# Optimization experiments

Hardware: AMD Instinct MI355X
Metric: run time of the kernel (lower is better)

## Reference

```python
import jax, jax.numpy as jnp
import numpy as np

C = 64
DQK = C // 8  # query/key channels


def setup_inputs() -> dict:
    key = jax.random.key(0)
    ks = jax.random.split(key, 8)
    B, H, W = 4, 64, 64
    x = jax.random.normal(ks[0], (B, C, H, W), dtype=jnp.float32)
    # 1x1 conv weights stored as (out_ch, in_ch); biases as (out_ch,)
    wq = jax.random.normal(ks[1], (DQK, C), dtype=jnp.float32) * 0.05
    bq = jnp.zeros((DQK,), dtype=jnp.float32)
    wk = jax.random.normal(ks[2], (DQK, C), dtype=jnp.float32) * 0.05
    bk = jnp.zeros((DQK,), dtype=jnp.float32)
    wv = jax.random.normal(ks[3], (C, C), dtype=jnp.float32) * 0.05
    bv = jnp.zeros((C,), dtype=jnp.float32)
    gamma = jnp.zeros((1,), dtype=jnp.float32)
    return {"x": x, "wq": wq, "bq": bq, "wk": wk, "bk": bk,
            "wv": wv, "bv": bv, "gamma": gamma}


def reference(x, wq, bq, wk, bk, wv, bv, gamma):
    B, Cc, H, W = x.shape
    N = H * W
    xf = x.reshape(B, Cc, N)  # (B, C, N)
    # 1x1 convs == channel-wise matmuls
    q = jnp.einsum('oc,bcn->bon', wq, xf) + bq[None, :, None]  # (B, dqk, N)
    k = jnp.einsum('oc,bcn->bon', wk, xf) + bk[None, :, None]  # (B, dqk, N)
    v = jnp.einsum('oc,bcn->bon', wv, xf) + bv[None, :, None]  # (B, C, N)
    # qk = q^T k -> (B, N, N), softmax over last dim
    qk = jnp.einsum('bdn,bdm->bnm', q, k)
    attn = jax.nn.softmax(qk, axis=-1)
    # out = v @ attn^T : out[b,c,i] = sum_j v[b,c,j] * attn[b,i,j]
    out = jnp.einsum('bcj,bij->bci', v, attn)
    out = out.reshape(B, Cc, H, W)
    return gamma * out + x
```

## Files before the change

kernel.cpp:

```cpp
#include <hip/hip_runtime.h>
#include <cmath>

namespace {

constexpr int B = 4;
constexpr int C = 64;
constexpr int N = 4096;
constexpr float LOG2E = 1.4426950408889634f;

typedef __bf16 bf16x8 __attribute__((ext_vector_type(8)));
typedef float f32x16 __attribute__((ext_vector_type(16)));
typedef unsigned short u16;

union B8 {
  int4 i;
  bf16x8 h;
  unsigned int w[4];
};

__device__ inline u16 f2bf(float f) {
  unsigned int u = __float_as_uint(f);
  u += 0x7FFFu + ((u >> 16) & 1u);
  return (u16)(u >> 16);
}

__device__ inline unsigned int cvt_pk_bf16(float lo, float hi) {
  unsigned int r;
  asm("v_cvt_pk_bf16_f32 %0, %1, %2" : "=v"(r) : "v"(lo), "v"(hi));
  return r;
}

__device__ inline float exp2_fast(float x) {
#if __has_builtin(__builtin_amdgcn_exp2f)
  return __builtin_amdgcn_exp2f(x);
#else
  return exp2f(x);
#endif
}

__device__ inline void pl32_swap(unsigned int& a, unsigned int& b) {
#if __has_builtin(__builtin_amdgcn_permlane32_swap)
  auto r = __builtin_amdgcn_permlane32_swap(a, b, false, false);
  a = (unsigned int)r[0];
  b = (unsigned int)r[1];
#else
  asm volatile("s_nop 1\n\tv_permlane32_swap_b32 %0, %1" : "+v"(a), "+v"(b));
#endif
}

__global__ __launch_bounds__(256) void qkv_kernel(
    const float* __restrict__ x,
    const float* __restrict__ wq, const float* __restrict__ bq,
    const float* __restrict__ wk, const float* __restrict__ bk,
    const float* __restrict__ wv, const float* __restrict__ bv,
    u16* __restrict__ qt, u16* __restrict__ kt, u16* __restrict__ vo) {
  const int bid = blockIdx.x;
  const int xcd = bid & 7;
  const int b = xcd >> 1;
  const int cg = (bid >> 3) & 3;
  const int nt = (xcd & 1) * 32 + (bid >> 5);
  const int t = threadIdx.x;
  const int nn = t & 63;
  const int wid = __builtin_amdgcn_readfirstlane(t >> 6);
  const int n = nt * 64 + nn;
  const float* xb = x + (size_t)b * C * N + n;

  const int c0 = cg * 16 + wid * 4;
  float a0 = bv[c0], a1 = bv[c0 + 1], a2 = bv[c0 + 2], a3 = bv[c0 + 3];

  if (cg == 0) {
    const int o0 = wid * 2;
    float qa0 = bq[o0], qa1 = bq[o0 + 1];
    float ka0 = bk[o0], ka1 = bk[o0 + 1];
    #pragma unroll 8
    for (int c = 0; c < C; ++c) {
      const float xv = xb[(size_t)c * N];
      a0 = fmaf(wv[(c0 + 0) * C + c], xv, a0);
      a1 = fmaf(wv[(c0 + 1) * C + c], xv, a1);
      a2 = fmaf(wv[(c0 + 2) * C + c], xv, a2);
      a3 = fmaf(wv[(c0 + 3) * C + c], xv, a3);
      qa0 = fmaf(wq[o0 * C + c], xv, qa0);
      qa1 = fmaf(wq[(o0 + 1) * C + c], xv, qa1);
      ka0 = fmaf(wk[o0 * C + c], xv, ka0);
      ka1 = fmaf(wk[(o0 + 1) * C + c], xv, ka1);
    }
    const unsigned int qw =
        (unsigned int)f2bf(qa0 * LOG2E) | ((unsigned int)f2bf(qa1 * LOG2E) << 16);
    const unsigned int kw =
        (unsigned int)f2bf(ka0) | ((unsigned int)f2bf(ka1) << 16);
    *reinterpret_cast<unsigned int*>(qt + ((size_t)b * N + n) * 8 + o0) = qw;
    *reinterpret_cast<unsigned int*>(kt + ((size_t)b * N + n) * 8 + o0) = kw;
  } else {
    #pragma unroll 8
    for (int c = 0; c < C; ++c) {
      const float xv = xb[(size_t)c * N];
      a0 = fmaf(wv[(c0 + 0) * C + c], xv, a0);
      a1 = fmaf(wv[(c0 + 1) * C + c], xv, a1);
      a2 = fmaf(wv[(c0 + 2) * C + c], xv, a2);
      a3 = fmaf(wv[(c0 + 3) * C + c], xv, a3);
    }
  }

  const size_t tb = ((size_t)b * (N / 16) + (n >> 4)) * (C * 16) + (n & 15);
  vo[tb + (size_t)(c0 + 0) * 16] = f2bf(a0);
  vo[tb + (size_t)(c0 + 1) * 16] = f2bf(a1);
  vo[tb + (size_t)(c0 + 2) * 16] = f2bf(a2);
  vo[tb + (size_t)(c0 + 3) * 16] = f2bf(a3);
}

__global__ __launch_bounds__(512, 4) void attn_kernel(
    const u16* __restrict__ qt, const u16* __restrict__ kt,
    const u16* __restrict__ vv, const float* __restrict__ x,
    const float* __restrict__ gamma, float* __restrict__ out) {
  const int bid = blockIdx.x;
  const int xcd = bid & 7;
  const int b = xcd >> 1;
  const int i0 = ((xcd & 1) * 64 + (bid >> 3)) * 32;
  const int t = threadIdx.x;
  const int lane = t & 63;
  const int w = __builtin_amdgcn_readfirstlane(t >> 6);
  const int il = lane & 31;
  const int hi = lane >> 5;

  __shared__ float l_lds[8][32];
  __shared__ u16 o_lds[8][32][66];

  B8 qf;
  if (hi == 0)
    qf.i = *reinterpret_cast<const int4*>(qt + ((size_t)b * N + i0 + il) * 8);
  else
    qf.i = make_int4(0, 0, 0, 0);

  const u16* ktb = kt + (size_t)b * N * 8;
  const u16* vbase = vv + (size_t)b * (N / 16) * (C * 16) + il * 16 + hi * 8;

  f32x16 accA, accB, zero16;
  #pragma unroll
  for (int r = 0; r < 16; ++r) { accA[r] = 0.f; accB[r] = 0.f; zero16[r] = 0.f; }
  float lrun = 0.f;

  B8 kfA, va0A, va1A, vb0A, vb1A;
  B8 kfB, va0B, va1B, vb0B, vb1B;

  auto LOAD = [&](int jt, B8& kf, B8& va0, B8& va1, B8& vb0, B8& vb1) {
    const int j0 = w * 512 + jt * 32;
    if (hi == 0)
      kf.i = *reinterpret_cast<const int4*>(ktb + (size_t)(j0 + il) * 8);
    else
      kf.i = make_int4(0, 0, 0, 0);
    const u16* vp = vbase + (size_t)(j0 >> 4) * (C * 16);
    va0.i = *reinterpret_cast<const int4*>(vp);
    va1.i = *reinterpret_cast<const int4*>(vp + 1024);
    vb0.i = *reinterpret_cast<const int4*>(vp + 512);
    vb1.i = *reinterpret_cast<const int4*>(vp + 1536);
  };

  auto COMPUTE = [&](const B8& kf, const B8& va0, const B8& va1, const B8& vb0,
                     const B8& vb1) {
    f32x16 S = __builtin_amdgcn_mfma_f32_32x32x16_bf16(kf.h, qf.h, zero16, 0, 0, 0);
    float p[16];
    #pragma unroll
    for (int r = 0; r < 16; ++r) p[r] = exp2_fast(S[r]);
    const float t0 = (p[0] + p[1]) + (p[2] + p[3]);
    const float t1 = (p[4] + p[5]) + (p[6] + p[7]);
    const float t2 = (p[8] + p[9]) + (p[10] + p[11]);
    const float t3 = (p[12] + p[13]) + (p[14] + p[15]);
    lrun += (t0 + t1) + (t2 + t3);
    B8 pf0, pf1;
    {
      unsigned a0 = cvt_pk_bf16(p[0], p[1]);
      unsigned a1 = cvt_pk_bf16(p[2], p[3]);
      unsigned b0 = cvt_pk_bf16(p[4], p[5]);
      unsigned b1 = cvt_pk_bf16(p[6], p[7]);
      pl32_swap(a0, b0);
      pl32_swap(a1, b1);
      pf0.w[0] = a0; pf0.w[1] = a1; pf0.w[2] = b0; pf0.w[3] = b1;
      a0 = cvt_pk_bf16(p[8], p[9]);
      a1 = cvt_pk_bf16(p[10], p[11]);
      b0 = cvt_pk_bf16(p[12], p[13]);
      b1 = cvt_pk_bf16(p[14], p[15]);
      pl32_swap(a0, b0);
      pl32_swap(a1, b1);
      pf1.w[0] = a0; pf1.w[1] = a1; pf1.w[2] = b0; pf1.w[3] = b1;
    }
    accA = __builtin_amdgcn_mfma_f32_32x32x16_bf16(va0.h, pf0.h, accA, 0, 0, 0);
    accA = __builtin_amdgcn_mfma_f32_32x32x16_bf16(va1.h, pf1.h, accA, 0, 0, 0);
    accB = __builtin_amdgcn_mfma_f32_32x32x16_bf16(vb0.h, pf0.h, accB, 0, 0, 0);
    accB = __builtin_amdgcn_mfma_f32_32x32x16_bf16(vb1.h, pf1.h, accB, 0, 0, 0);
  };

  LOAD(0, kfA, va0A, va1A, vb0A, vb1A);
  #pragma unroll 1
  for (int it = 0; it < 8; ++it) {
    LOAD(2 * it + 1, kfB, va0B, va1B, vb0B, vb1B);
    COMPUTE(kfA, va0A, va1A, vb0A, vb1A);
    if (it < 7) LOAD(2 * it + 2, kfA, va0A, va1A, vb0A, vb1A);
    COMPUTE(kfB, va0B, va1B, vb0B, vb1B);
  }

  const float lw = lrun + __shfl_xor(lrun, 32);
  if (hi == 0) l_lds[w][il] = lw;
  #pragma unroll
  for (int r = 0; r < 16; r += 2) {
    const int c = (r & 3) + 8 * (r >> 2) + 4 * hi;
    *reinterpret_cast<unsigned int*>(&o_lds[w][il][c]) =
        cvt_pk_bf16(accA[r], accA[r + 1]);
    *reinterpret_cast<unsigned int*>(&o_lds[w][il][c + 32]) =
        cvt_pk_bf16(accB[r], accB[r + 1]);
  }
  __syncthreads();

  const int i = t & 31;
  float Li = 0.f;
  #pragma unroll
  for (int ww = 0; ww < 8; ++ww) Li += l_lds[ww][i];
  const float ginv = gamma[0] / Li;

  #pragma unroll
  for (int q4 = 0; q4 < 4; ++q4) {
    const int flat = t + q4 * 512;
    const int c = flat >> 5;
    float s = 0.f;
    #pragma unroll
    for (int ww = 0; ww < 8; ++ww)
      s += __uint_as_float((unsigned int)o_lds[ww][i][c] << 16);
    const size_t off = ((size_t)b * C + c) * N + i0 + i;
    out[off] = fmaf(ginv, s, x[off]);
  }
}

}

extern "C" void kernel_launch(void* const* d_in, const int* in_sizes, int n_in,
                              void* d_out, int out_size, void* d_ws, size_t ws_size,
                              hipStream_t stream) {
  const float* x     = (const float*)d_in[0];
  const float* wq    = (const float*)d_in[1];
  const float* bq    = (const float*)d_in[2];
  const float* wk    = (const float*)d_in[3];
  const float* bk    = (const float*)d_in[4];
  const float* wv    = (const float*)d_in[5];
  const float* bv    = (const float*)d_in[6];
  const float* gamma = (const float*)d_in[7];
  float* out = (float*)d_out;

  u16* qt = (u16*)d_ws;
  u16* kt = qt + (size_t)B * N * 8;
  u16* vo = kt + (size_t)B * N * 8;

  qkv_kernel<<<B * 64 * 4, 256, 0, stream>>>(x, wq, bq, wk, bk, wv, bv, qt, kt, vo);
  attn_kernel<<<B * (N / 32), 512, 0, stream>>>(qt, kt, vo, x, gamma, out);
}
```

Before: 30.15 us.

## Software-pipeline QK MFMA one tile ahead of softmax and PV in attention loop

Restructures the attention inner loop so the score MFMA for tile j+1 is issued before the exp/pack and PV MFMAs of tile j. K is now loaded two tiles ahead, while V is loaded only within the current iteration instead of being double-buffered. The aim is to overlap MFMA latency with the exp2 and permlane work. The cost is that V loads now sit right before their use, which may expose memory latency, though register pressure is lower.

```diff
diff --git a/kernel.cpp b/kernel.cpp
--- a/kernel.cpp
+++ b/kernel.cpp
@@ -131,71 +131,80 @@
   else
     qf.i = make_int4(0, 0, 0, 0);
 
-  const u16* ktb = kt + (size_t)b * N * 8;
-  const u16* vbase = vv + (size_t)b * (N / 16) * (C * 16) + il * 16 + hi * 8;
+  const u16* kbase = kt + (size_t)b * N * 8 + ((size_t)w * 512 + il) * 8;
+  const u16* vbase = vv + (size_t)b * (N / 16) * (C * 16) +
+                     (size_t)w * 32 * (C * 16) + il * 16 + hi * 8;
 
   f32x16 accA, accB, zero16;
   #pragma unroll
   for (int r = 0; r < 16; ++r) { accA[r] = 0.f; accB[r] = 0.f; zero16[r] = 0.f; }
   float lrun = 0.f;
 
-  B8 kfA, va0A, va1A, vb0A, vb1A;
-  B8 kfB, va0B, va1B, vb0B, vb1B;
-
-  auto LOAD = [&](int jt, B8& kf, B8& va0, B8& va1, B8& vb0, B8& vb1) {
-    const int j0 = w * 512 + jt * 32;
+  B8 kfA, kfB, va0, va1, vb0, vb1;
+  f32x16 SA, SB;
+
+  auto LOADK = [&](int jt, B8& kf) {
     if (hi == 0)
-      kf.i = *reinterpret_cast<const int4*>(ktb + (size_t)(j0 + il) * 8);
+      kf.i = *reinterpret_cast<const int4*>(kbase + jt * 256);
     else
       kf.i = make_int4(0, 0, 0, 0);
-    const u16* vp = vbase + (size_t)(j0 >> 4) * (C * 16);
+  };
+  auto LOADV = [&](int jt) {
+    const u16* vp = vbase + jt * 2048;
     va0.i = *reinterpret_cast<const int4*>(vp);
     va1.i = *reinterpret_cast<const int4*>(vp + 1024);
     vb0.i = *reinterpret_cast<const int4*>(vp + 512);
     vb1.i = *reinterpret_cast<const int4*>(vp + 1536);
   };
 
-  auto COMPUTE = [&](const B8& kf, const B8& va0, const B8& va1, const B8& vb0,
-                     const B8& vb1) {
-    f32x16 S = __builtin_amdgcn_mfma_f32_32x32x16_bf16(kf.h, qf.h, zero16, 0, 0, 0);
-    float p[16];
-    #pragma unroll
-    for (int r = 0; r < 16; ++r) p[r] = exp2_fast(S[r]);
-    const float t0 = (p[0] + p[1]) + (p[2] + p[3]);
-    const float t1 = (p[4] + p[5]) + (p[6] + p[7]);
-    const float t2 = (p[8] + p[9]) + (p[10] + p[11]);
-    const float t3 = (p[12] + p[13]) + (p[14] + p[15]);
-    lrun += (t0 + t1) + (t2 + t3);
-    B8 pf0, pf1;
+  auto SMPACK = [&](const f32x16& S, B8& pf0, B8& pf1) {
     {
-      unsigned a0 = cvt_pk_bf16(p[0], p[1]);
-      unsigned a1 = cvt_pk_bf16(p[2], p[3]);
-      unsigned b0 = cvt_pk_bf16(p[4], p[5]);
-      unsigned b1 = cvt_pk_bf16(p[6], p[7]);
+      const float e0 = exp2_fast(S[0]), e1 = exp2_fast(S[1]);
+      const float e2 = exp2_fast(S[2]), e3 = exp2_fast(S[3]);
+      const float e4 = exp2_fast(S[4]), e5 = exp2_fast(S[5]);
+      const float e6 = exp2_fast(S[6]), e7 = exp2_fast(S[7]);
+      lrun += ((e0 + e1) + (e2 + e3)) + ((e4 + e5) + (e6 + e7));
+      unsigned a0 = cvt_pk_bf16(e0, e1), a1 = cvt_pk_bf16(e2, e3);
+      unsigned b0 = cvt_pk_bf16(e4, e5), b1 = cvt_pk_bf16(e6, e7);
       pl32_swap(a0, b0);
       pl32_swap(a1, b1);
       pf0.w[0] = a0; pf0.w[1] = a1; pf0.w[2] = b0; pf0.w[3] = b1;
-      a0 = cvt_pk_bf16(p[8], p[9]);
-      a1 = cvt_pk_bf16(p[10], p[11]);
-      b0 = cvt_pk_bf16(p[12], p[13]);
-      b1 = cvt_pk_bf16(p[14], p[15]);
+    }
+    {
+      const float e0 = exp2_fast(S[8]), e1 = exp2_fast(S[9]);
+      const float e2 = exp2_fast(S[10]), e3 = exp2_fast(S[11]);
+      const float e4 = exp2_fast(S[12]), e5 = exp2_fast(S[13]);
+      const float e6 = exp2_fast(S[14]), e7 = exp2_fast(S[15]);
+      lrun += ((e0 + e1) + (e2 + e3)) + ((e4 + e5) + (e6 + e7));
+      unsigned a0 = cvt_pk_bf16(e0, e1), a1 = cvt_pk_bf16(e2, e3);
+      unsigned b0 = cvt_pk_bf16(e4, e5), b1 = cvt_pk_bf16(e6, e7);
       pl32_swap(a0, b0);
       pl32_swap(a1, b1);
       pf1.w[0] = a0; pf1.w[1] = a1; pf1.w[2] = b0; pf1.w[3] = b1;
     }
+  };
+
+  auto BODY = [&](int jt, f32x16& Scur, f32x16& Snext, B8& Knext, B8& Kfree) {
+    if (jt + 1 < 16)
+      Snext = __builtin_amdgcn_mfma_f32_32x32x16_bf16(Knext.h, qf.h, zero16, 0, 0, 0);
+    if (jt + 2 < 16) LOADK(jt + 2, Kfree);
+    LOADV(jt);
+    B8 pf0, pf1;
+    SMPACK(Scur, pf0, pf1);
     accA = __builtin_amdgcn_mfma_f32_32x32x16_bf16(va0.h, pf0.h, accA, 0, 0, 0);
     accA = __builtin_amdgcn_mfma_f32_32x32x16_bf16(va1.h, pf1.h, accA, 0, 0, 0);
     accB = __builtin_amdgcn_mfma_f32_32x32x16_bf16(vb0.h, pf0.h, accB, 0, 0, 0);
     accB = __builtin_amdgcn_mfma_f32_32x32x16_bf16(vb1.h, pf1.h, accB, 0, 0, 0);
   };
 
-  LOAD(0, kfA, va0A, va1A, vb0A, vb1A);
+  LOADK(0, kfA);
+  SA = __builtin_amdgcn_mfma_f32_32x32x16_bf16(kfA.h, qf.h, zero16, 0, 0, 0);
+  LOADK(1, kfB);
+
   #pragma unroll 1
   for (int it = 0; it < 8; ++it) {
-    LOAD(2 * it + 1, kfB, va0B, va1B, vb0B, vb1B);
-    COMPUTE(kfA, va0A, va1A, vb0A, vb1A);
-    if (it < 7) LOAD(2 * it + 2, kfA, va0A, va1A, vb0A, vb1A);
-    COMPUTE(kfB, va0B, va1B, vb0B, vb1B);
+    BODY(2 * it, SA, SB, kfB, kfA);
+    BODY(2 * it + 1, SB, SA, kfA, kfB);
   }
 
   const float lw = lrun + __shfl_xor(lrun, 32);
```

New measurement: 30.12 us. About the same (-0.1%).
